# Kernel tuning notes

Measured on AMD Instinct MI355X. Metric: run time of the kernel, lower is better.

The kernel has to match this reference:

```python
import jax, jax.numpy as jnp
import numpy as np

B, N, D, IN_NF, OUT_NF, H, L = 64, 64, 3, 8, 1, 128, 4
BN = B * N
E = B * N * N


def setup_inputs() -> dict:
    key = jax.random.key(0)
    ks = jax.random.split(key, 12)
    g = lambda k, shape, s=0.05: jax.random.normal(k, shape, jnp.float32) * s
    z = lambda *shape: jnp.zeros(shape, jnp.float32)
    return {
        "xh": jax.random.normal(ks[0], (B, N, D + IN_NF), jnp.float32),
        "node_mask": jnp.ones((B, N, 1), jnp.float32),
        "edge_mask": jnp.ones((B, N * N, 1), jnp.float32),
        "emb_w": g(ks[1], (IN_NF, H)), "emb_b": z(H),
        "out_w": g(ks[2], (H, OUT_NF)), "out_b": z(OUT_NF),
        "ew1": g(ks[3], (L, 2 * H + 2, H)), "eb1": z(L, H),
        "ew2": g(ks[4], (L, H, H)), "eb2": z(L, H),
        "nw1": g(ks[5], (L, 2 * H, H)), "nb1": z(L, H),
        "nw2": g(ks[6], (L, H, H)), "nb2": z(L, H),
        "cw1": g(ks[7], (L, H, H)), "cb1": z(L, H),
        "cw2": g(ks[8], (L, H, 1), 0.001),  # xavier gain 0.001, no bias
    }


def _edges():
    # fully-connected edges within each graph block (matches get_adj_matrix)
    ii = jnp.repeat(jnp.arange(N, dtype=jnp.int32), N)  # source i
    jj = jnp.tile(jnp.arange(N, dtype=jnp.int32), N)    # target j
    offs = (jnp.arange(B, dtype=jnp.int32) * N)[:, None]
    row = (offs + ii[None, :]).reshape(-1)  # [E]
    col = (offs + jj[None, :]).reshape(-1)  # [E]
    return row, col


def reference(xh, node_mask, edge_mask, emb_w, emb_b, out_w, out_b,
              ew1, eb1, ew2, eb2, nw1, nb1, nw2, nb2, cw1, cb1, cw2):
    silu = jax.nn.silu
    row, col = _edges()
    nm = node_mask.reshape(BN, 1)
    em = edge_mask.reshape(E, 1)

    x = xh[:, :, :D].reshape(BN, D) * nm           # coordinates
    h = xh[:, :, D:].reshape(BN, IN_NF) * nm       # node features
    # static per-graph edge attribute: squared distance at input coords
    edge_attr = jnp.sum((x[row] - x[col]) ** 2, axis=1, keepdims=True)  # [E,1]

    h = h @ emb_w + emb_b  # embedding

    for l in range(L):
        coord_diff = x[row] - x[col]                            # [E,D]
        radial = jnp.sum(coord_diff ** 2, axis=1, keepdims=True)  # [E,1]
        coord_diff = coord_diff / (jnp.sqrt(radial + 1e-8) + 1.0)  # norm_diff

        # edge MLP: cat(h_i, h_j, radial, edge_attr) -> SiLU stack
        e_in = jnp.concatenate([h[row], h[col], radial, edge_attr], axis=1)
        m = silu(silu(e_in @ ew1[l] + eb1[l]) @ ew2[l] + eb2[l])  # [E,H]
        m = m * em

        # coordinate update (tanh=False): coord_diff * coord_mlp(m)
        trans = coord_diff * (silu(m @ cw1[l] + cb1[l]) @ cw2[l])  # [E,D]
        trans = trans * em
        x = x + jax.ops.segment_sum(trans, row, num_segments=BN)

        # node update with residual (recurrent=True)
        agg = jax.ops.segment_sum(m, row, num_segments=BN)       # [BN,H]
        n_in = jnp.concatenate([h, agg], axis=1)
        h = h + (silu(n_in @ nw1[l] + nb1[l]) @ nw2[l] + nb2[l])
        h = h * nm

    h = (h @ out_w + out_b) * nm                    # embedding_out + node mask
    return h.reshape(B, N, OUT_NF).mean(axis=1)     # [B, out_nf]
```

## Files before the change

### kernel.cpp

```cpp
#include <hip/hip_runtime.h>
#include <math.h>


#define NB 64
#define NN 64
#define DD 3
#define INNF 8
#define HH 128
#define LL 4
#define BNODES (NB * NN)

typedef __attribute__((ext_vector_type(8))) short bf16x8;
typedef __attribute__((ext_vector_type(4))) float f32x4;
typedef __attribute__((ext_vector_type(4))) unsigned uint32x4;

__device__ __forceinline__ float silu_f(float v) {
    float e = __expf(-v);
    return v * __builtin_amdgcn_rcpf(1.0f + e);
}

__device__ __forceinline__ short f2bf(float v) {
    unsigned u = __builtin_bit_cast(unsigned, v);
    u += 0x7fffu + ((u >> 16) & 1u);
    return (short)(u >> 16);
}

__device__ __forceinline__ unsigned cvt_pk2(float lo, float hi) {
    unsigned r;
    asm("v_cvt_pk_bf16_f32 %0, %1, %2" : "=v"(r) : "v"(lo), "v"(hi));
    return r;
}

__global__ void prep_kernel(const float* __restrict__ xh, const float* __restrict__ nm,
                            const float* __restrict__ emb_w, const float* __restrict__ emb_b,
                            float* __restrict__ x, float* __restrict__ x0, float* __restrict__ h) {
    const int v = blockIdx.x;
    const int t = threadIdx.x;
    const float m = nm[v];
    __shared__ float f[INNF];
    if (t < INNF) f[t] = xh[v * (DD + INNF) + DD + t] * m;
    if (t < DD) {
        float c = xh[v * (DD + INNF) + t] * m;
        x[v * DD + t] = c;
        x0[v * DD + t] = c;
    }
    __syncthreads();
    float acc = emb_b[t];
#pragma unroll
    for (int k = 0; k < INNF; ++k) acc = fmaf(f[k], emb_w[k * HH + t], acc);
    h[v * HH + t] = acc;
}

__global__ void wprep_kernel(const float* __restrict__ ew1, const float* __restrict__ ew2,
                             const float* __restrict__ cw1, const float* __restrict__ nw1,
                             const float* __restrict__ nw2,
                             short* __restrict__ ew1T, short* __restrict__ ew2T,
                             short* __restrict__ cw1T, short* __restrict__ nw1T,
                             short* __restrict__ nw2T) {
    const int l = blockIdx.x / 5, which = blockIdx.x % 5;
    if (which == 0) {
        const float* src = ew1 + (size_t)l * 258 * HH;
        short* dst = ew1T + (size_t)l * 256 * HH;
        for (int idx = threadIdx.x; idx < 256 * HH; idx += blockDim.x) {
            const int cp = idx >> 7, k = idx & 127;
            dst[cp * HH + k] = f2bf(src[(k + ((cp >> 7) << 7)) * HH + (cp & 127)]);
        }
    } else if (which == 3) {
        const float* src = nw1 + (size_t)l * 2 * HH * HH;
        short* dst = nw1T + (size_t)l * 2 * HH * HH;
        for (int idx = threadIdx.x; idx < 2 * HH * HH; idx += blockDim.x) {
            const int c = idx >> 8, k = idx & 255;
            dst[c * 256 + k] = f2bf(src[k * HH + c]);
        }
    } else {
        const float* src = (which == 1 ? ew2 : which == 2 ? cw1 : nw2) + (size_t)l * HH * HH;
        short* dst = (which == 1 ? ew2T : which == 2 ? cw1T : nw2T) + (size_t)l * HH * HH;
        for (int idx = threadIdx.x; idx < HH * HH; idx += blockDim.x) {
            const int k = idx >> 7, c = idx & 127;
            dst[c * HH + k] = f2bf(src[idx]);
        }
    }
}

__global__ __launch_bounds__(256) void pq_kernel(const float* __restrict__ h,
                                                 const short* __restrict__ ew1Tl,
                                                 const float* __restrict__ eb1l,
                                                 float* __restrict__ P, float* __restrict__ Q) {
    const int gph = blockIdx.x & 63;
    const int g0n = gph * NN + ((blockIdx.x >> 6) & 3) * 16;
    const int half = blockIdx.x >> 8;
    const int t = threadIdx.x;
    const int w = t >> 6, l = t & 63, l15 = l & 15, l4 = l >> 4;
    __shared__ __align__(16) char shN[16 * 256];

    {
        const int row = t >> 4, k0 = (t & 15) * 8;
        const float* hp = h + (size_t)(g0n + row) * HH + k0;
        const float4 a = *(const float4*)hp;
        const float4 b = *(const float4*)(hp + 4);
        uint32x4 s;
        s[0] = cvt_pk2(a.x, a.y);
        s[1] = cvt_pk2(a.z, a.w);
        s[2] = cvt_pk2(b.x, b.y);
        s[3] = cvt_pk2(b.z, b.w);
        *(uint32x4*)(shN + row * 256 + ((k0 * 2) ^ ((row & 7) << 4))) = s;
    }
    __syncthreads();

    const int c0 = half * 128 + w * 32;
    f32x4 acc[2];
    acc[0] = (f32x4){0.f, 0.f, 0.f, 0.f};
    acc[1] = (f32x4){0.f, 0.f, 0.f, 0.f};
#pragma unroll
    for (int kt = 0; kt < 4; ++kt) {
        const bf16x8 af = *(const bf16x8*)(shN + l15 * 256 + (((kt * 4 + l4) * 16) ^ ((l15 & 7) << 4)));
#pragma unroll
        for (int ct2 = 0; ct2 < 2; ++ct2) {
            const bf16x8 bf = *(const bf16x8*)(ew1Tl + (size_t)(c0 + ct2 * 16 + l15) * HH + kt * 32 + l4 * 8);
            acc[ct2] = __builtin_amdgcn_mfma_f32_16x16x32_bf16(af, bf, acc[ct2], 0, 0, 0);
        }
    }
#pragma unroll
    for (int ct2 = 0; ct2 < 2; ++ct2) {
        const int cp = c0 + ct2 * 16 + l15;
        const int c = cp & 127;
        float* dst = (cp >= HH) ? Q : P;
        const float bias = (cp >= HH) ? 0.0f : eb1l[c];
#pragma unroll
        for (int reg = 0; reg < 4; ++reg) {
            const int n = g0n + l4 * 4 + reg;
            dst[(size_t)n * HH + c] = acc[ct2][reg] + bias;
        }
    }
}

__global__ __launch_bounds__(256, 4) void edge_kernel(
    const float* __restrict__ P, const float* __restrict__ Q,
    const float* __restrict__ x, const float* __restrict__ x0,
    const float* __restrict__ em,
    const float* __restrict__ ew1l,
    const short* __restrict__ ew2T,
    const float* __restrict__ eb2l,
    const short* __restrict__ cw1T,
    const float* __restrict__ cb1l,
    const float* __restrict__ cw2l,
    float* __restrict__ x_out, float* __restrict__ agg) {

    const int g  = blockIdx.x & 63;
    const int ii = blockIdx.x >> 6;
    const int iA = ii, iB = ii + 32;
    const int g0 = g * NN;
    const int rA = g0 + iA, rB = g0 + iB;
    const int t = threadIdx.x;
    const int w = t >> 6;
    const int l = t & 63;
    const int l15 = l & 15, l4 = l >> 4;
    const int c0 = w * 32;

    __shared__ __align__(16) char shAc[128 * 256];
    float* shphiP = (float*)(shAc);
    float* shx0g  = (float*)(shAc + 2048);
    __shared__ float shPA[HH], shPB[HH], shw256[HH], shw257[HH];
    __shared__ float shEb2[HH], shCb1[HH], shCw2[HH];
    __shared__ float shx[NN * 3];
    __shared__ float shradA[NN], shradB[NN], sheaA[NN], sheaB[NN], shemA[NN], shemB[NN];
    __shared__ float shcdnA[NN * 3], shcdnB[NN * 3];

    if (t < HH) {
        shPA[t] = P[rA * HH + t];
        shPB[t] = P[rB * HH + t];
        shw256[t] = ew1l[256 * HH + t];
        shw257[t] = ew1l[257 * HH + t];
        shEb2[t] = eb2l[t];
        shCb1[t] = cb1l[t];
        shCw2[t] = cw2l[t];
    }
    if (t < NN * 3) {
        shx[t] = x[g0 * 3 + t];
        shx0g[t] = x0[g0 * 3 + t];
    }
    __syncthreads();
    if (t < 2 * NN) {
        const int j = t & 63;
        const bool isB = (t >= NN);
        const int ni = isB ? iB : iA;
        float dx = shx[ni * 3 + 0] - shx[j * 3 + 0];
        float dy = shx[ni * 3 + 1] - shx[j * 3 + 1];
        float dz = shx[ni * 3 + 2] - shx[j * 3 + 2];
        float rad = dx * dx + dy * dy + dz * dz;
        float inv = 1.0f / (sqrtf(rad + 1e-8f) + 1.0f);
        float ex = shx0g[ni * 3 + 0] - shx0g[j * 3 + 0];
        float ey = shx0g[ni * 3 + 1] - shx0g[j * 3 + 1];
        float ez = shx0g[ni * 3 + 2] - shx0g[j * 3 + 2];
        float ea = ex * ex + ey * ey + ez * ez;
        float* radp = isB ? shradB : shradA;
        float* eap  = isB ? sheaB : sheaA;
        float* emp  = isB ? shemB : shemA;
        float* cdnp = isB ? shcdnB : shcdnA;
        radp[j] = rad;
        eap[j] = ea;
        emp[j] = em[(isB ? rB : rA) * NN + j];
        cdnp[j * 3 + 0] = dx * inv;
        cdnp[j * 3 + 1] = dy * inv;
        cdnp[j * 3 + 2] = dz * inv;
    }
    __syncthreads();

    {
        const int j = t >> 2;
        const float radA = shradA[j], eaA = sheaA[j];
        const float radB = shradB[j], eaB = sheaB[j];
        const int xr = (j & 7) << 4;
        float4 qbuf[8];
#pragma unroll
        for (int p = 0; p < 4; ++p) {
            const int k0 = (t & 3) * 8 + p * 32;
            qbuf[2 * p]     = *(const float4*)(Q + (size_t)(g0 + j) * HH + k0);
            qbuf[2 * p + 1] = *(const float4*)(Q + (size_t)(g0 + j) * HH + k0 + 4);
        }
#pragma unroll
        for (int p = 0; p < 4; ++p) {
            const int k0 = (t & 3) * 8 + p * 32;
            const float4 qa = qbuf[2 * p];
            const float4 qb = qbuf[2 * p + 1];
            const float qv[8] = {qa.x, qa.y, qa.z, qa.w, qb.x, qb.y, qb.z, qb.w};
            uint32x4 sA, sB;
#pragma unroll
            for (int u2 = 0; u2 < 4; ++u2) {
                const int ka = k0 + 2 * u2, kb = ka + 1;
                const float w2a = shw256[ka], w3a = shw257[ka];
                const float w2b = shw256[kb], w3b = shw257[kb];
                float vA0 = silu_f(shPA[ka] + qv[2 * u2] + radA * w2a + eaA * w3a);
                float vA1 = silu_f(shPA[kb] + qv[2 * u2 + 1] + radA * w2b + eaA * w3b);
                float vB0 = silu_f(shPB[ka] + qv[2 * u2] + radB * w2a + eaB * w3a);
                float vB1 = silu_f(shPB[kb] + qv[2 * u2 + 1] + radB * w2b + eaB * w3b);
                sA[u2] = cvt_pk2(vA0, vA1);
                sB[u2] = cvt_pk2(vB0, vB1);
            }
            const int off = (k0 * 2) ^ xr;
            *(uint32x4*)(shAc + j * 256 + off) = sA;
            *(uint32x4*)(shAc + (j + 64) * 256 + off) = sB;
        }
    }
    __syncthreads();

    f32x4 acc[8][2];
#pragma unroll
    for (int rt = 0; rt < 8; ++rt) {
        acc[rt][0] = (f32x4){0.f, 0.f, 0.f, 0.f};
        acc[rt][1] = (f32x4){0.f, 0.f, 0.f, 0.f};
    }
    {
        const short* B2 = ew2T + (size_t)(c0 + l15) * HH + l4 * 8;
        bf16x8 bcur[2], bnxt[2];
        bcur[0] = *(const bf16x8*)(B2);
        bcur[1] = *(const bf16x8*)(B2 + 16 * HH);
        __builtin_amdgcn_s_setprio(1);
#pragma unroll
        for (int kt = 0; kt < 4; ++kt) {
            if (kt < 3) {
                bnxt[0] = *(const bf16x8*)(B2 + (kt + 1) * 32);
                bnxt[1] = *(const bf16x8*)(B2 + 16 * HH + (kt + 1) * 32);
            }
            bf16x8 af[8];
#pragma unroll
            for (int rt = 0; rt < 8; ++rt) {
                const int row = rt * 16 + l15;
                af[rt] = *(const bf16x8*)(shAc + row * 256 + (((kt * 4 + l4) * 16) ^ ((row & 7) << 4)));
            }
#pragma unroll
            for (int rt = 0; rt < 8; ++rt) {
                acc[rt][0] = __builtin_amdgcn_mfma_f32_16x16x32_bf16(af[rt], bcur[0], acc[rt][0], 0, 0, 0);
                acc[rt][1] = __builtin_amdgcn_mfma_f32_16x16x32_bf16(af[rt], bcur[1], acc[rt][1], 0, 0, 0);
            }
            bcur[0] = bnxt[0];
            bcur[1] = bnxt[1];
        }
        __builtin_amdgcn_s_setprio(0);
    }
    __syncthreads();

#pragma unroll
    for (int ct2 = 0; ct2 < 2; ++ct2) {
        const int c = c0 + ct2 * 16 + l15;
        const float b = shEb2[c];
        float paggA = 0.0f, paggB = 0.0f;
#pragma unroll
        for (int rt = 0; rt < 8; ++rt) {
            const int rbase = rt * 16 + l4 * 4;
            float v[4];
#pragma unroll
            for (int reg = 0; reg < 4; ++reg) {
                const int row = rbase + reg;
                const float emv = (rt < 4) ? shemA[row] : shemB[row - 64];
                v[reg] = silu_f(acc[rt][ct2][reg] + b) * emv;
                if (rt < 4) paggA += v[reg]; else paggB += v[reg];
            }
            const unsigned wlo = cvt_pk2(v[0], v[1]);
            const unsigned whi = cvt_pk2(v[2], v[3]);
            const int cx = c * 2;
#pragma unroll
            for (int reg = 0; reg < 4; ++reg) {
                const int row = rbase + reg;
                const unsigned wv = (reg < 2) ? wlo : whi;
                const short sv = (reg & 1) ? (short)(wv >> 16) : (short)(wv & 0xffff);
                *(short*)(shAc + row * 256 + (cx ^ ((row & 7) << 4))) = sv;
            }
        }
        paggA += __shfl_xor(paggA, 16);
        paggA += __shfl_xor(paggA, 32);
        paggB += __shfl_xor(paggB, 16);
        paggB += __shfl_xor(paggB, 32);
        if (l4 == 0) {
            agg[rA * HH + c] = paggA;
            agg[rB * HH + c] = paggB;
        }
    }
    __syncthreads();

#pragma unroll
    for (int rt = 0; rt < 8; ++rt) {
        acc[rt][0] = (f32x4){0.f, 0.f, 0.f, 0.f};
        acc[rt][1] = (f32x4){0.f, 0.f, 0.f, 0.f};
    }
    {
        const short* B3 = cw1T + (size_t)(c0 + l15) * HH + l4 * 8;
        bf16x8 bcur[2], bnxt[2];
        bcur[0] = *(const bf16x8*)(B3);
        bcur[1] = *(const bf16x8*)(B3 + 16 * HH);
        __builtin_amdgcn_s_setprio(1);
#pragma unroll
        for (int kt = 0; kt < 4; ++kt) {
            if (kt < 3) {
                bnxt[0] = *(const bf16x8*)(B3 + (kt + 1) * 32);
                bnxt[1] = *(const bf16x8*)(B3 + 16 * HH + (kt + 1) * 32);
            }
            bf16x8 af[8];
#pragma unroll
            for (int rt = 0; rt < 8; ++rt) {
                const int row = rt * 16 + l15;
                af[rt] = *(const bf16x8*)(shAc + row * 256 + (((kt * 4 + l4) * 16) ^ ((row & 7) << 4)));
            }
#pragma unroll
            for (int rt = 0; rt < 8; ++rt) {
                acc[rt][0] = __builtin_amdgcn_mfma_f32_16x16x32_bf16(af[rt], bcur[0], acc[rt][0], 0, 0, 0);
                acc[rt][1] = __builtin_amdgcn_mfma_f32_16x16x32_bf16(af[rt], bcur[1], acc[rt][1], 0, 0, 0);
            }
            bcur[0] = bnxt[0];
            bcur[1] = bnxt[1];
        }
        __builtin_amdgcn_s_setprio(0);
    }

    float pp[8][4];
    {
#pragma unroll
        for (int rt = 0; rt < 8; ++rt)
#pragma unroll
            for (int reg = 0; reg < 4; ++reg) pp[rt][reg] = 0.0f;
#pragma unroll
        for (int ct2 = 0; ct2 < 2; ++ct2) {
            const int c = c0 + ct2 * 16 + l15;
            const float cb = shCb1[c], cw = shCw2[c];
#pragma unroll
            for (int rt = 0; rt < 8; ++rt) {
#pragma unroll
                for (int reg = 0; reg < 4; ++reg) {
                    float v = silu_f(acc[rt][ct2][reg] + cb);
                    pp[rt][reg] = fmaf(v, cw, pp[rt][reg]);
                }
            }
        }
#pragma unroll
        for (int off = 8; off >= 1; off >>= 1) {
#pragma unroll
            for (int rt = 0; rt < 8; ++rt)
#pragma unroll
                for (int reg = 0; reg < 4; ++reg) pp[rt][reg] += __shfl_xor(pp[rt][reg], off);
        }
    }
    __syncthreads();
    if (l15 == 0) {
#pragma unroll
        for (int rt = 0; rt < 8; ++rt)
#pragma unroll
            for (int reg = 0; reg < 4; ++reg)
                shphiP[w * 128 + rt * 16 + l4 * 4 + reg] = pp[rt][reg];
    }
    __syncthreads();

    if (t < 192) {
        const int q = t >> 6, j = t & 63;
        float phiA = shphiP[0 * 128 + j] + shphiP[1 * 128 + j] + shphiP[2 * 128 + j] + shphiP[3 * 128 + j];
        float vA = shcdnA[j * 3 + q] * phiA * shemA[j];
        float phiB = shphiP[0 * 128 + 64 + j] + shphiP[1 * 128 + 64 + j] + shphiP[2 * 128 + 64 + j] + shphiP[3 * 128 + 64 + j];
        float vB = shcdnB[j * 3 + q] * phiB * shemB[j];
#pragma unroll
        for (int off = 32; off >= 1; off >>= 1) {
            vA += __shfl_xor(vA, off);
            vB += __shfl_xor(vB, off);
        }
        if (j == 0) {
            x_out[rA * 3 + q] = shx[iA * 3 + q] + vA;
            x_out[rB * 3 + q] = shx[iB * 3 + q] + vB;
        }
    }
}

__global__ __launch_bounds__(256) void nodepq_kernel(
    float* __restrict__ h, const float* __restrict__ agg, const float* __restrict__ nm,
    const short* __restrict__ nw1Tl, const float* __restrict__ nb1l,
    const short* __restrict__ nw2Tl, const float* __restrict__ nb2l,
    const short* __restrict__ ew1Tn, const float* __restrict__ eb1n,
    float* __restrict__ P, float* __restrict__ Q, int do_pq) {
    const int g0n = (blockIdx.x & 63) * NN + (blockIdx.x >> 6) * 16;
    const int t = threadIdx.x;
    const int w = t >> 6, l = t & 63, l15 = l & 15, l4 = l >> 4;
    __shared__ __align__(16) char shN[16 * 512];
    __shared__ __align__(16) char shT[16 * 256];
    char* shH = shN;

    {
        const int row = t >> 4, k0 = (t & 15) * 16;
        const float* src = (k0 < HH) ? (h + (size_t)(g0n + row) * HH + k0)
                                     : (agg + (size_t)(g0n + row) * HH + (k0 - HH));
        const float4 a = *(const float4*)src;
        const float4 b = *(const float4*)(src + 4);
        const float4 c = *(const float4*)(src + 8);
        const float4 d = *(const float4*)(src + 12);
        uint32x4 s0, s1;
        s0[0] = cvt_pk2(a.x, a.y); s0[1] = cvt_pk2(a.z, a.w);
        s0[2] = cvt_pk2(b.x, b.y); s0[3] = cvt_pk2(b.z, b.w);
        s1[0] = cvt_pk2(c.x, c.y); s1[1] = cvt_pk2(c.z, c.w);
        s1[2] = cvt_pk2(d.x, d.y); s1[3] = cvt_pk2(d.z, d.w);
        const int xr = (row & 7) << 4;
        *(uint32x4*)(shN + row * 512 + ((k0 * 2) ^ xr)) = s0;
        *(uint32x4*)(shN + row * 512 + ((k0 * 2 + 16) ^ xr)) = s1;
    }
    __syncthreads();

    const int c0 = w * 32;
    f32x4 acc[2];
    acc[0] = (f32x4){0.f, 0.f, 0.f, 0.f};
    acc[1] = (f32x4){0.f, 0.f, 0.f, 0.f};
#pragma unroll
    for (int kt = 0; kt < 8; ++kt) {
        const bf16x8 af = *(const bf16x8*)(shN + l15 * 512 + (((kt * 4 + l4) * 16) ^ ((l15 & 7) << 4)));
#pragma unroll
        for (int ct2 = 0; ct2 < 2; ++ct2) {
            const bf16x8 bf = *(const bf16x8*)(nw1Tl + (size_t)(c0 + ct2 * 16 + l15) * 256 + kt * 32 + l4 * 8);
            acc[ct2] = __builtin_amdgcn_mfma_f32_16x16x32_bf16(af, bf, acc[ct2], 0, 0, 0);
        }
    }
    __syncthreads();
#pragma unroll
    for (int ct2 = 0; ct2 < 2; ++ct2) {
        const int c = c0 + ct2 * 16 + l15;
        const float b = nb1l[c];
        float v[4];
#pragma unroll
        for (int reg = 0; reg < 4; ++reg) v[reg] = silu_f(acc[ct2][reg] + b);
        const unsigned wlo = cvt_pk2(v[0], v[1]);
        const unsigned whi = cvt_pk2(v[2], v[3]);
#pragma unroll
        for (int reg = 0; reg < 4; ++reg) {
            const int row = l4 * 4 + reg;
            const unsigned wv = (reg < 2) ? wlo : whi;
            const short sv = (reg & 1) ? (short)(wv >> 16) : (short)(wv & 0xffff);
            *(short*)(shT + row * 256 + ((c * 2) ^ ((row & 7) << 4))) = sv;
        }
    }
    __syncthreads();

    acc[0] = (f32x4){0.f, 0.f, 0.f, 0.f};
    acc[1] = (f32x4){0.f, 0.f, 0.f, 0.f};
#pragma unroll
    for (int kt = 0; kt < 4; ++kt) {
        const bf16x8 af = *(const bf16x8*)(shT + l15 * 256 + (((kt * 4 + l4) * 16) ^ ((l15 & 7) << 4)));
#pragma unroll
        for (int ct2 = 0; ct2 < 2; ++ct2) {
            const bf16x8 bf = *(const bf16x8*)(nw2Tl + (size_t)(c0 + ct2 * 16 + l15) * HH + kt * 32 + l4 * 8);
            acc[ct2] = __builtin_amdgcn_mfma_f32_16x16x32_bf16(af, bf, acc[ct2], 0, 0, 0);
        }
    }
    float hn[2][4];
#pragma unroll
    for (int ct2 = 0; ct2 < 2; ++ct2) {
        const int c = c0 + ct2 * 16 + l15;
        const float b = nb2l[c];
#pragma unroll
        for (int reg = 0; reg < 4; ++reg) {
            const int n = g0n + l4 * 4 + reg;
            const float hv = h[(size_t)n * HH + c];
            hn[ct2][reg] = (hv + acc[ct2][reg] + b) * nm[n];
            h[(size_t)n * HH + c] = hn[ct2][reg];
        }
    }
    if (!do_pq) return;

#pragma unroll
    for (int ct2 = 0; ct2 < 2; ++ct2) {
        const int c = c0 + ct2 * 16 + l15;
        const unsigned wlo = cvt_pk2(hn[ct2][0], hn[ct2][1]);
        const unsigned whi = cvt_pk2(hn[ct2][2], hn[ct2][3]);
#pragma unroll
        for (int reg = 0; reg < 4; ++reg) {
            const int row = l4 * 4 + reg;
            const unsigned wv = (reg < 2) ? wlo : whi;
            const short sv = (reg & 1) ? (short)(wv >> 16) : (short)(wv & 0xffff);
            *(short*)(shH + row * 256 + ((c * 2) ^ ((row & 7) << 4))) = sv;
        }
    }
    __syncthreads();

    f32x4 pacc[2][2];
#pragma unroll
    for (int half = 0; half < 2; ++half) {
        pacc[half][0] = (f32x4){0.f, 0.f, 0.f, 0.f};
        pacc[half][1] = (f32x4){0.f, 0.f, 0.f, 0.f};
    }
#pragma unroll
    for (int kt = 0; kt < 4; ++kt) {
        const bf16x8 af = *(const bf16x8*)(shH + l15 * 256 + (((kt * 4 + l4) * 16) ^ ((l15 & 7) << 4)));
#pragma unroll
        for (int half = 0; half < 2; ++half) {
#pragma unroll
            for (int ct2 = 0; ct2 < 2; ++ct2) {
                const bf16x8 bf = *(const bf16x8*)(ew1Tn + (size_t)(half * 128 + c0 + ct2 * 16 + l15) * HH + kt * 32 + l4 * 8);
                pacc[half][ct2] = __builtin_amdgcn_mfma_f32_16x16x32_bf16(af, bf, pacc[half][ct2], 0, 0, 0);
            }
        }
    }
#pragma unroll
    for (int half = 0; half < 2; ++half) {
#pragma unroll
        for (int ct2 = 0; ct2 < 2; ++ct2) {
            const int cp = half * 128 + c0 + ct2 * 16 + l15;
            const int c = cp & 127;
            float* dst = (cp >= HH) ? Q : P;
            const float bias = (cp >= HH) ? 0.0f : eb1n[c];
#pragma unroll
            for (int reg = 0; reg < 4; ++reg) {
                const int n = g0n + l4 * 4 + reg;
                dst[(size_t)n * HH + c] = pacc[half][ct2][reg] + bias;
            }
        }
    }
}

__global__ void out_kernel(const float* __restrict__ h, const float* __restrict__ nm,
                           const float* __restrict__ ow, const float* __restrict__ ob,
                           float* __restrict__ out) {
    const int b = blockIdx.x;
    const int n = threadIdx.x;
    const int v = b * NN + n;
    float acc = 0.0f;
#pragma unroll 8
    for (int c = 0; c < HH; ++c) acc = fmaf(h[v * HH + c], ow[c], acc);
    acc = (acc + ob[0]) * nm[v];
#pragma unroll
    for (int off = 32; off >= 1; off >>= 1) acc += __shfl_xor(acc, off);
    if (n == 0) out[b] = acc * (1.0f / (float)NN);
}

extern "C" void kernel_launch(void* const* d_in, const int* in_sizes, int n_in,
                              void* d_out, int out_size, void* d_ws, size_t ws_size,
                              hipStream_t stream) {
    const float* xh    = (const float*)d_in[0];
    const float* nmask = (const float*)d_in[1];
    const float* emask = (const float*)d_in[2];
    const float* emb_w = (const float*)d_in[3];
    const float* emb_b = (const float*)d_in[4];
    const float* out_w = (const float*)d_in[5];
    const float* out_b = (const float*)d_in[6];
    const float* ew1   = (const float*)d_in[7];
    const float* eb1   = (const float*)d_in[8];
    const float* ew2   = (const float*)d_in[9];
    const float* eb2   = (const float*)d_in[10];
    const float* nw1   = (const float*)d_in[11];
    const float* nb1   = (const float*)d_in[12];
    const float* nw2   = (const float*)d_in[13];
    const float* nb2   = (const float*)d_in[14];
    const float* cw1   = (const float*)d_in[15];
    const float* cb1   = (const float*)d_in[16];
    const float* cw2   = (const float*)d_in[17];

    float* ws  = (float*)d_ws;
    float* xA  = ws;
    float* xB  = xA + BNODES * 3;
    float* x0  = xB + BNODES * 3;
    float* h   = x0 + BNODES * 3;
    float* Pb  = h + BNODES * HH;
    float* Qb  = Pb + BNODES * HH;
    float* agg = Qb + BNODES * HH;
    short* ew2T = (short*)(agg + BNODES * HH);
    short* cw1T = ew2T + LL * HH * HH;
    short* ew1T = cw1T + LL * HH * HH;
    short* nw1T = ew1T + LL * 256 * HH;
    short* nw2T = nw1T + LL * 256 * HH;

    prep_kernel<<<BNODES, HH, 0, stream>>>(xh, nmask, emb_w, emb_b, xA, x0, h);
    wprep_kernel<<<5 * LL, 256, 0, stream>>>(ew1, ew2, cw1, nw1, nw2,
                                             ew1T, ew2T, cw1T, nw1T, nw2T);

    pq_kernel<<<512, 256, 0, stream>>>(h, ew1T, eb1, Pb, Qb);

    float* xc = xA;
    float* xn = xB;
    for (int l = 0; l < LL; ++l) {
        const float* ew1l = ew1 + (size_t)l * 258 * HH;
        edge_kernel<<<BNODES / 2, 256, 0, stream>>>(Pb, Qb, xc, x0, emask, ew1l,
                                                    ew2T + (size_t)l * HH * HH, eb2 + l * HH,
                                                    cw1T + (size_t)l * HH * HH, cb1 + l * HH,
                                                    cw2 + (size_t)l * HH, xn, agg);
        const int do_pq = (l + 1 < LL) ? 1 : 0;
        const int ln = do_pq ? (l + 1) : 0;
        nodepq_kernel<<<256, 256, 0, stream>>>(h, agg, nmask,
                                               nw1T + (size_t)l * 2 * HH * HH, nb1 + l * HH,
                                               nw2T + (size_t)l * HH * HH, nb2 + l * HH,
                                               ew1T + (size_t)ln * 256 * HH, eb1 + ln * HH,
                                               Pb, Qb, do_pq);
        float* tmp = xc; xc = xn; xn = tmp;
    }

    out_kernel<<<NB, NN, 0, stream>>>(h, nmask, out_w, out_b, (float*)d_out);
}
```

Before: 255.6 us.

## Fuse node embedding into first PQ kernel and inline edge geometry in edge kernel

Replaces the per-node prep kernel with a small coordinate-only prep, and computes the node embedding (h = masked features @ emb_w + emb_b) directly inside the first P/Q projection kernel, which also writes h out from one half of the blocks. In the edge kernel, the separate pass that precomputed radial, edge_attr and normalized coord diffs into shared memory (followed by a barrier) is removed. Each thread now recomputes those values in registers, and one lane in four writes the shared cdn/mask arrays. This removes a launch, a global round trip for h, and one __syncthreads. In exchange the embedding is computed redundantly in both halves of the grid and the geometry math is duplicated across lanes.

```diff
diff --git a/kernel.cpp b/kernel.cpp
--- a/kernel.cpp
+++ b/kernel.cpp
@@ -31,24 +31,15 @@
     return r;
 }
 
-__global__ void prep_kernel(const float* __restrict__ xh, const float* __restrict__ nm,
-                            const float* __restrict__ emb_w, const float* __restrict__ emb_b,
-                            float* __restrict__ x, float* __restrict__ x0, float* __restrict__ h) {
-    const int v = blockIdx.x;
-    const int t = threadIdx.x;
-    const float m = nm[v];
-    __shared__ float f[INNF];
-    if (t < INNF) f[t] = xh[v * (DD + INNF) + DD + t] * m;
-    if (t < DD) {
-        float c = xh[v * (DD + INNF) + t] * m;
-        x[v * DD + t] = c;
-        x0[v * DD + t] = c;
-    }
-    __syncthreads();
-    float acc = emb_b[t];
-#pragma unroll
-    for (int k = 0; k < INNF; ++k) acc = fmaf(f[k], emb_w[k * HH + t], acc);
-    h[v * HH + t] = acc;
+__global__ void xprep_kernel(const float* __restrict__ xh, const float* __restrict__ nm,
+                             float* __restrict__ x, float* __restrict__ x0) {
+    const int idx = blockIdx.x * 256 + threadIdx.x;
+    if (idx < BNODES * 3) {
+        const int v = idx / 3, q = idx - v * 3;
+        const float c = xh[v * (DD + INNF) + q] * nm[v];
+        x[idx] = c;
+        x0[idx] = c;
+    }
 }
 
 __global__ void wprep_kernel(const float* __restrict__ ew1, const float* __restrict__ ew2,
@@ -82,10 +73,14 @@
     }
 }
 
-__global__ __launch_bounds__(256) void pq_kernel(const float* __restrict__ h,
-                                                 const short* __restrict__ ew1Tl,
-                                                 const float* __restrict__ eb1l,
-                                                 float* __restrict__ P, float* __restrict__ Q) {
+__global__ __launch_bounds__(256) void pq0_kernel(const float* __restrict__ xh,
+                                                  const float* __restrict__ nm,
+                                                  const float* __restrict__ emb_w,
+                                                  const float* __restrict__ emb_b,
+                                                  const short* __restrict__ ew1Tl,
+                                                  const float* __restrict__ eb1l,
+                                                  float* __restrict__ P, float* __restrict__ Q,
+                                                  float* __restrict__ hout) {
     const int gph = blockIdx.x & 63;
     const int g0n = gph * NN + ((blockIdx.x >> 6) & 3) * 16;
     const int half = blockIdx.x >> 8;
@@ -95,14 +90,26 @@
 
     {
         const int row = t >> 4, k0 = (t & 15) * 8;
-        const float* hp = h + (size_t)(g0n + row) * HH + k0;
-        const float4 a = *(const float4*)hp;
-        const float4 b = *(const float4*)(hp + 4);
+        const int n = g0n + row;
+        const float m = nm[n];
+        float hv[8];
+#pragma unroll
+        for (int c = 0; c < 8; ++c) hv[c] = emb_b[k0 + c];
+#pragma unroll
+        for (int k = 0; k < INNF; ++k) {
+            const float f = xh[(size_t)n * (DD + INNF) + DD + k] * m;
+#pragma unroll
+            for (int c = 0; c < 8; ++c) hv[c] = fmaf(f, emb_w[k * HH + k0 + c], hv[c]);
+        }
+        if (half == 0) {
+            *(float4*)(hout + (size_t)n * HH + k0) = (float4){hv[0], hv[1], hv[2], hv[3]};
+            *(float4*)(hout + (size_t)n * HH + k0 + 4) = (float4){hv[4], hv[5], hv[6], hv[7]};
+        }
         uint32x4 s;
-        s[0] = cvt_pk2(a.x, a.y);
-        s[1] = cvt_pk2(a.z, a.w);
-        s[2] = cvt_pk2(b.x, b.y);
-        s[3] = cvt_pk2(b.z, b.w);
+        s[0] = cvt_pk2(hv[0], hv[1]);
+        s[1] = cvt_pk2(hv[2], hv[3]);
+        s[2] = cvt_pk2(hv[4], hv[5]);
+        s[3] = cvt_pk2(hv[6], hv[7]);
         *(uint32x4*)(shN + row * 256 + ((k0 * 2) ^ ((row & 7) << 4))) = s;
     }
     __syncthreads();
@@ -159,11 +166,10 @@
 
     __shared__ __align__(16) char shAc[128 * 256];
     float* shphiP = (float*)(shAc);
-    float* shx0g  = (float*)(shAc + 2048);
     __shared__ float shPA[HH], shPB[HH], shw256[HH], shw257[HH];
     __shared__ float shEb2[HH], shCb1[HH], shCw2[HH];
-    __shared__ float shx[NN * 3];
-    __shared__ float shradA[NN], shradB[NN], sheaA[NN], sheaB[NN], shemA[NN], shemB[NN];
+    __shared__ float shx[NN * 3], shx0g[NN * 3];
+    __shared__ float shemA[NN], shemB[NN];
     __shared__ float shcdnA[NN * 3], shcdnB[NN * 3];
 
     if (t < HH) {
@@ -180,36 +186,31 @@
         shx0g[t] = x0[g0 * 3 + t];
     }
     __syncthreads();
-    if (t < 2 * NN) {
-        const int j = t & 63;
-        const bool isB = (t >= NN);
-        const int ni = isB ? iB : iA;
-        float dx = shx[ni * 3 + 0] - shx[j * 3 + 0];
-        float dy = shx[ni * 3 + 1] - shx[j * 3 + 1];
-        float dz = shx[ni * 3 + 2] - shx[j * 3 + 2];
-        float rad = dx * dx + dy * dy + dz * dz;
-        float inv = 1.0f / (sqrtf(rad + 1e-8f) + 1.0f);
-        float ex = shx0g[ni * 3 + 0] - shx0g[j * 3 + 0];
-        float ey = shx0g[ni * 3 + 1] - shx0g[j * 3 + 1];
-        float ez = shx0g[ni * 3 + 2] - shx0g[j * 3 + 2];
-        float ea = ex * ex + ey * ey + ez * ez;
-        float* radp = isB ? shradB : shradA;
-        float* eap  = isB ? sheaB : sheaA;
-        float* emp  = isB ? shemB : shemA;
-        float* cdnp = isB ? shcdnB : shcdnA;
-        radp[j] = rad;
-        eap[j] = ea;
-        emp[j] = em[(isB ? rB : rA) * NN + j];
-        cdnp[j * 3 + 0] = dx * inv;
-        cdnp[j * 3 + 1] = dy * inv;
-        cdnp[j * 3 + 2] = dz * inv;
-    }
-    __syncthreads();
 
     {
         const int j = t >> 2;
-        const float radA = shradA[j], eaA = sheaA[j];
-        const float radB = shradB[j], eaB = sheaB[j];
+        const float xjx = shx[j * 3 + 0], xjy = shx[j * 3 + 1], xjz = shx[j * 3 + 2];
+        const float dxA = shx[iA * 3 + 0] - xjx, dyA = shx[iA * 3 + 1] - xjy, dzA = shx[iA * 3 + 2] - xjz;
+        const float dxB = shx[iB * 3 + 0] - xjx, dyB = shx[iB * 3 + 1] - xjy, dzB = shx[iB * 3 + 2] - xjz;
+        const float radA = dxA * dxA + dyA * dyA + dzA * dzA;
+        const float radB = dxB * dxB + dyB * dyB + dzB * dzB;
+        const float x0jx = shx0g[j * 3 + 0], x0jy = shx0g[j * 3 + 1], x0jz = shx0g[j * 3 + 2];
+        const float exA = shx0g[iA * 3 + 0] - x0jx, eyA = shx0g[iA * 3 + 1] - x0jy, ezA = shx0g[iA * 3 + 2] - x0jz;
+        const float exB = shx0g[iB * 3 + 0] - x0jx, eyB = shx0g[iB * 3 + 1] - x0jy, ezB = shx0g[iB * 3 + 2] - x0jz;
+        const float eaA = exA * exA + eyA * eyA + ezA * ezA;
+        const float eaB = exB * exB + eyB * eyB + ezB * ezB;
+        if ((t & 3) == 0) {
+            const float invA = 1.0f / (sqrtf(radA + 1e-8f) + 1.0f);
+            const float invB = 1.0f / (sqrtf(radB + 1e-8f) + 1.0f);
+            shcdnA[j * 3 + 0] = dxA * invA;
+            shcdnA[j * 3 + 1] = dyA * invA;
+            shcdnA[j * 3 + 2] = dzA * invA;
+            shcdnB[j * 3 + 0] = dxB * invB;
+            shcdnB[j * 3 + 1] = dyB * invB;
+            shcdnB[j * 3 + 2] = dzB * invB;
+            shemA[j] = em[rA * NN + j];
+            shemB[j] = em[rB * NN + j];
+        }
         const int xr = (j & 7) << 4;
         float4 qbuf[8];
 #pragma unroll
@@ -599,11 +600,11 @@
     short* nw1T = ew1T + LL * 256 * HH;
     short* nw2T = nw1T + LL * 256 * HH;
 
-    prep_kernel<<<BNODES, HH, 0, stream>>>(xh, nmask, emb_w, emb_b, xA, x0, h);
+    xprep_kernel<<<48, 256, 0, stream>>>(xh, nmask, xA, x0);
     wprep_kernel<<<5 * LL, 256, 0, stream>>>(ew1, ew2, cw1, nw1, nw2,
                                              ew1T, ew2T, cw1T, nw1T, nw2T);
 
-    pq_kernel<<<512, 256, 0, stream>>>(h, ew1T, eb1, Pb, Qb);
+    pq0_kernel<<<512, 256, 0, stream>>>(xh, nmask, emb_w, emb_b, ew1T, eb1, Pb, Qb, h);
 
     float* xc = xA;
     float* xn = xB;
```

New measurement: 257.9 us. Within noise of the previous version (+0.9%).
